# Performance work log

Measured on AMD Instinct MI355X. Metric: run time of the kernel, lower is better.

The kernel has to match this reference:

```python
import jax, jax.numpy as jnp
import numpy as np

B, T, N, M = 64, 128, 128, 512


def setup_inputs() -> dict:
    key = jax.random.key(0)
    ks = jax.random.split(key, 9)
    w = 0.02
    return dict(
        X=jax.random.normal(ks[0], (B, T, N), jnp.float32),
        h0=jax.random.normal(ks[1], (B, M), jnp.float32) * 0.05,
        s0=jax.random.normal(ks[2], (B, M), jnp.float32) * 0.05,
        # LSTM cell params (keras gate order: i, f, c, o)
        W_lstm=jax.random.normal(ks[3], (N, 4 * M), jnp.float32) * w,
        U_lstm=jax.random.normal(ks[4], (M, 4 * M), jnp.float32) * w,
        b_lstm=jnp.zeros((4 * M,), jnp.float32),
        # InputAttention params: W_e: Dense(T) on concat([h,c]) (2m -> T),
        # U_e: Dense(T) on X^T (T -> T), v_e: Dense(1) (T -> 1)
        W_e=jax.random.normal(ks[5], (2 * M, T), jnp.float32) * w,
        b_We=jnp.zeros((T,), jnp.float32),
        U_e=jax.random.normal(ks[6], (T, T), jnp.float32) * w,
        b_Ue=jnp.zeros((T,), jnp.float32),
        v_e=jax.random.normal(ks[7], (T, 1), jnp.float32) * w,
        b_ve=jnp.zeros((1,), jnp.float32),
    )


def reference(X, h0, s0, W_lstm, U_lstm, b_lstm, W_e, b_We, U_e, b_Ue, v_e, b_ve):
    # In the original, every loop iteration t runs a single LSTM step on
    # X[:, t, :] starting from the SAME initial_state [h0, s0] (state is not
    # carried across t), so all T steps are independent -> vectorize over T.
    z = jnp.einsum('btn,nk->btk', X, W_lstm) + (h0 @ U_lstm + b_lstm)[:, None, :]
    zi, zf, zc, zo = jnp.split(z, 4, axis=-1)  # keras gate order i,f,c,o
    i = jax.nn.sigmoid(zi)
    f = jax.nn.sigmoid(zf)
    o = jax.nn.sigmoid(zo)
    c = f * s0[:, None, :] + i * jnp.tanh(zc)  # (B, T, m)
    h = o * jnp.tanh(c)                        # (B, T, m)

    # InputAttention for every t at once:
    # e_t = v_e(tanh(W_e([h_t; c_t]) broadcast over n  +  U_e(X^T)))
    hc = jnp.concatenate([h, c], axis=-1)              # (B, T, 2m)
    A = hc @ W_e + b_We                                # (B, T, T)
    U = jnp.einsum('btn,tk->bnk', X, U_e) + b_Ue       # (B, n, T)
    e = jnp.tanh(A[:, :, None, :] + U[:, None, :, :])  # (B, T, n, T)
    scores = jnp.einsum('btnk,k->btn', e, v_e[:, 0]) + b_ve[0]  # (B, T, n)
    alpha = jax.nn.softmax(scores, axis=-1)            # softmax over n
    return X * alpha
```

## Files before the change

kernel.cpp:

```cpp
#include <hip/hip_runtime.h>

typedef __attribute__((ext_vector_type(8))) short bfrag;
typedef __attribute__((ext_vector_type(4))) float f32x4;

#define C_SCALE 2.885390081777926815f

__device__ __forceinline__ float fast_rcp(float x){
#if __has_builtin(__builtin_amdgcn_rcpf)
  return __builtin_amdgcn_rcpf(x);
#else
  return 1.0f/x;
#endif
}
__device__ __forceinline__ float fexp2(float x){
#if __has_builtin(__builtin_amdgcn_exp2f)
  return __builtin_amdgcn_exp2f(x);
#else
  return exp2f(x);
#endif
}
__device__ __forceinline__ float sigm(float x){ return fast_rcp(1.0f + __expf(-x)); }
__device__ __forceinline__ float tanh_f(float x){ return 1.0f - 2.0f*fast_rcp(__expf(2.0f*x) + 1.0f); }
__device__ __forceinline__ unsigned short f2bf(float f){
  unsigned u = __float_as_uint(f);
  return (unsigned short)((u + 0x7fffu + ((u>>16)&1u)) >> 16);
}
__device__ __forceinline__ void gload16(const void* g, void* l){
  __builtin_amdgcn_global_load_lds((const __attribute__((address_space(1))) void*)g,
                                   (__attribute__((address_space(3))) void*)l, 16, 0, 0);
}

__global__ __launch_bounds__(256) void prep(const float* __restrict__ X,
                                            unsigned short* __restrict__ Xbf,
                                            const float* __restrict__ Wl,
                                            unsigned short* __restrict__ Wlt,
                                            const float* __restrict__ We,
                                            unsigned short* __restrict__ Wet,
                                            const float* __restrict__ h0,
                                            const float* __restrict__ Ul,
                                            float* __restrict__ Uhp,
                                            const float* __restrict__ Ue,
                                            const float* __restrict__ bUe,
                                            unsigned short* __restrict__ UTb){
  __shared__ __align__(16) float sh[6600];
  const int tid = threadIdx.x;
  const int bid = blockIdx.x;

  if (bid < 512){
    const int i = (bid*256 + tid)*8;
    float4 a = *(const float4*)&X[i];
    float4 b = *(const float4*)&X[i+4];
    ushort4 lo, hi;
    lo.x=f2bf(a.x); lo.y=f2bf(a.y); lo.z=f2bf(a.z); lo.w=f2bf(a.w);
    hi.x=f2bf(b.x); hi.y=f2bf(b.y); hi.z=f2bf(b.z); hi.w=f2bf(b.w);
    *(ushort4*)&Xbf[i] = lo; *(ushort4*)&Xbf[i+4] = hi;
  } else if (bid < 608){
    const float* in; unsigned short* outp; int K, N, j0, k0, perm;
    if (bid < 576){ int r = bid-512; in = Wl; outp = Wlt; K = 128;  N = 2048; j0 = (r&31)*64; k0 = (r>>5)*64; perm = 0; }
    else          { int r = bid-576; in = We; outp = Wet; K = 1024; N = 128;  j0 = (r&1)*64;  k0 = (r>>1)*64; perm = 1; }
    float (*t)[68] = (float(*)[68])sh;
#pragma unroll
    for (int i=0;i<4;i++){
      int idx = tid + i*256;
      int r = idx>>4, c4 = idx&15;
      int kk = k0 + r;
      int srow = perm ? ((kk&1) ? 512 + (kk>>1) : (kk>>1)) : kk;
      *(float4*)&t[r][c4*4] = *(const float4*)&in[srow*N + j0 + c4*4];
    }
    __syncthreads();
#pragma unroll
    for (int i=0;i<4;i++){
      int idx = tid + i*256;
      int r = idx>>4, c4 = idx&15;
      ushort4 o;
      o.x = f2bf(t[c4*4+0][r]); o.y = f2bf(t[c4*4+1][r]);
      o.z = f2bf(t[c4*4+2][r]); o.w = f2bf(t[c4*4+3][r]);
      *(ushort4*)&outp[(j0+r)*K + k0 + c4*4] = o;
    }
  } else if (bid < 736){
    const int r = bid - 608;
    const int nh = r & 1, b = r >> 1;
    float (*Xs)[68]  = (float(*)[68])sh;
    float (*Us)[132] = (float(*)[132])(sh + 2176);
    const int tc5 = tid & 31, tr8 = tid >> 5;
    f32x4 a4[8];
#pragma unroll
    for (int j=0;j<8;j++) a4[j] = (f32x4){0.f,0.f,0.f,0.f};
    for (int tk=0; tk<4; tk++){
#pragma unroll
      for (int i=0;i<2;i++){
        int idx = tid + i*256;
        int t = idx>>4, nq = idx&15;
        *(float4*)&Xs[t][nq*4] = *(const float4*)&X[(b*128 + tk*32 + t)*128 + nh*64 + nq*4];
      }
#pragma unroll
      for (int i=0;i<4;i++){
        int idx = tid + i*256;
        int t = idx>>5, kq = idx&31;
        *(float4*)&Us[t][kq*4] = *(const float4*)&Ue[(tk*32+t)*128 + kq*4];
      }
      __syncthreads();
#pragma unroll 4
      for (int t=0;t<32;t++){
        f32x4 u4 = *(const f32x4*)&Us[t][tc5*4];
        f32x4 x0 = *(const f32x4*)&Xs[t][tr8*8];
        f32x4 x1 = *(const f32x4*)&Xs[t][tr8*8+4];
        a4[0] += x0.x*u4; a4[1] += x0.y*u4; a4[2] += x0.z*u4; a4[3] += x0.w*u4;
        a4[4] += x1.x*u4; a4[5] += x1.y*u4; a4[6] += x1.z*u4; a4[7] += x1.w*u4;
      }
      __syncthreads();
    }
    const f32x4 bu = *(const f32x4*)&bUe[tc5*4];
#pragma unroll
    for (int j=0;j<8;j++){
      const int n = nh*64 + tr8*8 + j;
      f32x4 v = a4[j] + bu;
      ushort4 o;
      o.x = f2bf(fexp2(C_SCALE*v.x)); o.y = f2bf(fexp2(C_SCALE*v.y));
      o.z = f2bf(fexp2(C_SCALE*v.z)); o.w = f2bf(fexp2(C_SCALE*v.w));
      *(ushort4*)&UTb[(b*128 + n)*128 + tc5*4] = o;
    }
  } else {
    const int r = bid - 736;
    const int jc = r & 15;
    const int bc = (r>>4) >> 2, kc = (r>>4) & 3;
    float (*h0s)[128] = (float(*)[128])sh;
#pragma unroll
    for (int i=0;i<2;i++){
      int idx = tid + i*256;
      int bi = idx>>5, kq = idx&31;
      *(float4*)&h0s[bi][kq*4] = *(const float4*)&h0[(bc*16+bi)*512 + kc*128 + kq*4];
    }
    __syncthreads();
    const int jj = tid & 127, bh = tid >> 7;
    const int j = jc*128 + jj;
    float acc[8];
#pragma unroll
    for (int i=0;i<8;i++) acc[i]=0.f;
    for (int k=0;k<128;k+=4){
      float w0 = Ul[(kc*128+k+0)*2048 + j];
      float w1 = Ul[(kc*128+k+1)*2048 + j];
      float w2 = Ul[(kc*128+k+2)*2048 + j];
      float w3 = Ul[(kc*128+k+3)*2048 + j];
#pragma unroll
      for (int bi=0;bi<8;bi++){
        float4 h4 = *(const float4*)&h0s[bh*8+bi][k];
        acc[bi] += h4.x*w0 + h4.y*w1 + h4.z*w2 + h4.w*w3;
      }
    }
#pragma unroll
    for (int bi=0;bi<8;bi++)
      Uhp[kc*131072 + (bc*16 + bh*8 + bi)*2048 + j] = acc[bi];
  }
}

__global__ __launch_bounds__(256) void k2_mfma(const unsigned short* __restrict__ Xbf,
                                               const unsigned short* __restrict__ Wlt,
                                               const float* __restrict__ Uhp,
                                               const float* __restrict__ bl,
                                               const float* __restrict__ s0,
                                               unsigned int* __restrict__ hci){
  __shared__ __align__(16) char lds[65536];
  const int tid = threadIdx.x;
  const int mc = blockIdx.x;
  const int b  = blockIdx.y;
  const int bt0 = b*128;
  const int lane = tid & 63, wave = tid >> 6;
  const int wr = wave >> 1, wc = wave & 1;

#pragma unroll
  for (int i=0;i<8;i++){
    int g = tid + i*256;
    int r = g>>4, G = g&15;
    gload16(Xbf + (bt0+r)*128 + ((G ^ (r&7))<<3), lds + g*16);
  }
#pragma unroll
  for (int i=0;i<8;i++){
    int g = tid + i*256;
    int c = g>>4, G = g&15;
    int q = c>>4;
    int j = (q&3)*512 + mc*32 + ((q>>2)<<4) + (c&15);
    gload16(Wlt + j*128 + ((G ^ (c&7))<<3), lds + 32768 + g*16);
  }
  __syncthreads();

  f32x4 acc[4][4];
#pragma unroll
  for (int mt=0;mt<4;mt++)
#pragma unroll
    for (int nt=0;nt<4;nt++) acc[mt][nt] = (f32x4){0.f,0.f,0.f,0.f};

#pragma unroll
  for (int ks=0;ks<4;ks++){
    const int kb = ks*64 + ((lane>>4)<<4);
    bfrag a[4], bb[4];
#pragma unroll
    for (int mt=0;mt<4;mt++){
      int r = wr*64 + mt*16 + (lane&15);
      a[mt] = *(const bfrag*)&lds[r*256 + (kb ^ ((r&7)<<4))];
    }
#pragma unroll
    for (int nt=0;nt<4;nt++){
      int c = wc*64 + nt*16 + (lane&15);
      bb[nt] = *(const bfrag*)&lds[32768 + c*256 + (kb ^ ((c&7)<<4))];
    }
#pragma unroll
    for (int mt=0;mt<4;mt++)
#pragma unroll
      for (int nt=0;nt<4;nt++)
        acc[mt][nt] = __builtin_amdgcn_mfma_f32_16x16x32_bf16(a[mt], bb[nt], acc[mt][nt], 0, 0, 0);
  }

  const int mloc = mc*32 + wc*16 + (lane&15);
  float uh[4];
#pragma unroll
  for (int g=0;g<4;g++){
    int j = g*512 + mloc;
    uh[g] = bl[j] + Uhp[0*131072 + b*2048 + j] + Uhp[1*131072 + b*2048 + j]
                  + Uhp[2*131072 + b*2048 + j] + Uhp[3*131072 + b*2048 + j];
  }
  const float s0v = s0[b*512 + mloc];
#pragma unroll
  for (int mt=0;mt<4;mt++){
#pragma unroll
    for (int reg=0;reg<4;reg++){
      int row = wr*64 + mt*16 + (lane>>4)*4 + reg;
      float zi = acc[mt][0][reg] + uh[0];
      float zf = acc[mt][1][reg] + uh[1];
      float zc = acc[mt][2][reg] + uh[2];
      float zo = acc[mt][3][reg] + uh[3];
      float fi = sigm(zi), ff = sigm(zf), fo = sigm(zo);
      float cv = ff*s0v + fi*tanh_f(zc);
      float hv = fo*tanh_f(cv);
      hci[(bt0+row)*512 + mloc] = (unsigned)f2bf(hv) | ((unsigned)f2bf(cv) << 16);
    }
  }
}

__global__ __launch_bounds__(256) void k3_mfma(const unsigned short* __restrict__ hc,
                                               const unsigned short* __restrict__ Wet,
                                               const float* __restrict__ bWe,
                                               float* __restrict__ eA){
  __shared__ __align__(16) char lds[49152];
  const int tid = threadIdx.x;
  const int rc = blockIdx.x;
  const int bt0 = rc*64;
  const int lane = tid & 63, wave = tid >> 6;
  const int wr = wave >> 1, wc = wave & 1;

  f32x4 acc[2][4];
#pragma unroll
  for (int mt=0;mt<2;mt++)
#pragma unroll
    for (int nt=0;nt<4;nt++) acc[mt][nt] = (f32x4){0.f,0.f,0.f,0.f};

  for (int ks=0; ks<8; ks++){
    const int k0 = ks*128;
#pragma unroll
    for (int i=0;i<4;i++){
      int g = tid + i*256;
      int r = g>>4, G = g&15;
      gload16(hc + (bt0+r)*1024 + k0 + ((G ^ (r&7))<<3), lds + g*16);
    }
#pragma unroll
    for (int i=0;i<8;i++){
      int g = tid + i*256;
      int nn = g>>4, G = g&15;
      gload16(Wet + nn*1024 + k0 + ((G ^ (nn&7))<<3), lds + 16384 + g*16);
    }
    __syncthreads();
#pragma unroll
    for (int kk=0;kk<4;kk++){
      const int kb = kk*64 + ((lane>>4)<<4);
      bfrag a[2], bb[4];
#pragma unroll
      for (int mt=0;mt<2;mt++){
        int r = wr*32 + mt*16 + (lane&15);
        a[mt] = *(const bfrag*)&lds[r*256 + (kb ^ ((r&7)<<4))];
      }
#pragma unroll
      for (int nt=0;nt<4;nt++){
        int nn = wc*64 + nt*16 + (lane&15);
        bb[nt] = *(const bfrag*)&lds[16384 + nn*256 + (kb ^ ((nn&7)<<4))];
      }
#pragma unroll
      for (int mt=0;mt<2;mt++)
#pragma unroll
        for (int nt=0;nt<4;nt++)
          acc[mt][nt] = __builtin_amdgcn_mfma_f32_16x16x32_bf16(a[mt], bb[nt], acc[mt][nt], 0, 0, 0);
    }
    __syncthreads();
  }
#pragma unroll
  for (int mt=0;mt<2;mt++)
#pragma unroll
    for (int reg=0;reg<4;reg++){
      int row = wr*32 + mt*16 + (lane>>4)*4 + reg;
#pragma unroll
      for (int nt=0;nt<4;nt++){
        int col = wc*64 + nt*16 + (lane&15);
        eA[(bt0+row)*128 + col] = fexp2(C_SCALE*(acc[mt][nt][reg] + bWe[col]));
      }
    }
}

__global__ __launch_bounds__(256) void k5_score(const float* __restrict__ X,
                                                const unsigned short* __restrict__ UTb,
                                                const float* __restrict__ eA,
                                                const float* __restrict__ ve,
                                                float* __restrict__ out){
  __shared__ __align__(16) unsigned short Un[128*128];
  __shared__ __align__(16) float As[8*128];
  __shared__ __align__(16) float vs[128];
  __shared__ float redm[4][4], reds[4][4];
  const int tid = threadIdx.x;
  const int tch = blockIdx.x;
  const int b   = blockIdx.y;
  const int tpair = tid>>7, n = tid&127, wid = tid>>6;

  {
    const unsigned short* src = UTb + b*16384;
#pragma unroll
    for (int i=0;i<8;i++){
      int g = tid + i*256;
      int nn = g>>4, G = g&15;
      gload16(src + nn*128 + ((G ^ (nn&7))<<3), (char*)Un + g*16);
    }
    const float* asrc = eA + (b*128 + tch*8)*128;
    gload16(asrc + tid*4, (char*)As + tid*16);
    if (tid < 128) vs[tid] = ve[tid];
  }
  __syncthreads();

  f32x4 sc[4];
#pragma unroll
  for (int tt=0;tt<4;tt++) sc[tt] = (f32x4){0.f,0.f,0.f,0.f};

  const char* Urow = (const char*)Un + n*256;
  const int swz = (n&7)<<4;
#pragma unroll 4
  for (int k8=0; k8<16; k8++){
    uint4 u = *(const uint4*)(Urow + ((k8*16) ^ swz));
    f32x4 ua, ub;
    ua.x = __uint_as_float(u.x<<16); ua.y = __uint_as_float(u.x & 0xffff0000u);
    ua.z = __uint_as_float(u.y<<16); ua.w = __uint_as_float(u.y & 0xffff0000u);
    ub.x = __uint_as_float(u.z<<16); ub.y = __uint_as_float(u.z & 0xffff0000u);
    ub.z = __uint_as_float(u.w<<16); ub.w = __uint_as_float(u.w & 0xffff0000u);
    const f32x4 va = *(const f32x4*)&vs[k8*8];
    const f32x4 vb = *(const f32x4*)&vs[k8*8+4];
#pragma unroll
    for (int tt=0; tt<4; tt++){
      const float* Ar = &As[(tt*2+tpair)*128 + k8*8];
      f32x4 ea = *(const f32x4*)Ar;
      f32x4 eb = *(const f32x4*)(Ar+4);
      f32x4 ra, rb;
      ra.x = fast_rcp(ea.x*ua.x + 1.f); ra.y = fast_rcp(ea.y*ua.y + 1.f);
      ra.z = fast_rcp(ea.z*ua.z + 1.f); ra.w = fast_rcp(ea.w*ua.w + 1.f);
      rb.x = fast_rcp(eb.x*ub.x + 1.f); rb.y = fast_rcp(eb.y*ub.y + 1.f);
      rb.z = fast_rcp(eb.z*ub.z + 1.f); rb.w = fast_rcp(eb.w*ub.w + 1.f);
      sc[tt] += va*ra;
      sc[tt] += vb*rb;
    }
  }

  float sv[4];
#pragma unroll
  for (int tt=0;tt<4;tt++){
    float s = -2.f*((sc[tt].x + sc[tt].y) + (sc[tt].z + sc[tt].w));
    sv[tt] = s;
    float m = s;
#pragma unroll
    for (int off=32; off>0; off>>=1) m = fmaxf(m, __shfl_xor(m, off));
    if ((tid&63)==0) redm[wid][tt] = m;
  }
  __syncthreads();
  float evv[4];
#pragma unroll
  for (int tt=0;tt<4;tt++){
    const float M = fmaxf(redm[tpair*2][tt], redm[tpair*2+1][tt]);
    float e = __expf(sv[tt] - M);
    evv[tt] = e;
    float s = e;
#pragma unroll
    for (int off=32; off>0; off>>=1) s += __shfl_xor(s, off);
    if ((tid&63)==0) reds[wid][tt] = s;
  }
  __syncthreads();
#pragma unroll
  for (int tt=0;tt<4;tt++){
    const float S = reds[tpair*2][tt] + reds[tpair*2+1][tt];
    const float alpha = evv[tt] * fast_rcp(S);
    const int t = tch*8 + tt*2 + tpair;
    const int g = (b*128 + t)*128 + n;
    out[g] = X[g] * alpha;
  }
}

extern "C" void kernel_launch(void* const* d_in, const int* in_sizes, int n_in,
                              void* d_out, int out_size, void* d_ws, size_t ws_size,
                              hipStream_t stream){
  (void)in_sizes; (void)n_in; (void)out_size; (void)ws_size;
  const float* X   = (const float*)d_in[0];
  const float* h0  = (const float*)d_in[1];
  const float* s0  = (const float*)d_in[2];
  const float* Wl  = (const float*)d_in[3];
  const float* Ul  = (const float*)d_in[4];
  const float* bl  = (const float*)d_in[5];
  const float* We  = (const float*)d_in[6];
  const float* bWe = (const float*)d_in[7];
  const float* Ue  = (const float*)d_in[8];
  const float* bUe = (const float*)d_in[9];
  const float* ve  = (const float*)d_in[10];
  float* out = (float*)d_out;

  char* ws = (char*)d_ws;
  unsigned short* Wlt = (unsigned short*)(ws + 0);
  unsigned short* Wet = (unsigned short*)(ws + 524288);
  unsigned short* Xbf = (unsigned short*)(ws + 786432);
  unsigned short* UTb = (unsigned short*)(ws + 2883584);
  unsigned short* hc  = (unsigned short*)(ws + 4980736);
  float*          Uhp = (float*)(ws + 21757952);
  float*          eA  = (float*)(ws + 23855104);

  prep    <<<dim3(992),   256, 0, stream>>>(X, Xbf, Wl, Wlt, We, Wet, h0, Ul, Uhp, Ue, bUe, UTb);
  k2_mfma <<<dim3(16,64), 256, 0, stream>>>(Xbf, Wlt, Uhp, bl, s0, (unsigned int*)hc);
  k3_mfma <<<dim3(128),   256, 0, stream>>>(hc, Wet, bWe, eA);
  k5_score<<<dim3(16,64), 256, 0, stream>>>(X, UTb, eA, ve, out);
}
```

Before: 67.68 us.

## Shrink LDS footprints, split k3 tiles, retile UTb for direct global reads

k2 now stages the K dimension in two 64-wide halves, halving its LDS use, and launches on a flattened 1D grid. k3 is split into 512 smaller blocks, each computing a 32x64 output tile, so more blocks run across CUs. UTb is written in a k-tiled layout so k5 can read it with coalesced loads straight from global memory, dropping its 32KB LDS staging. The aim is higher occupancy and less LDS staging; the costs are extra barriers in k2, more redundant loads of hc and Wet in k3, and k5 now depending on cache hits for the repeated UTb reads.

```diff
diff --git a/kernel.cpp b/kernel.cpp
--- a/kernel.cpp
+++ b/kernel.cpp
@@ -111,6 +111,7 @@
       __syncthreads();
     }
     const f32x4 bu = *(const f32x4*)&bUe[tc5*4];
+    const int ktile = tc5 >> 1, khalf = tc5 & 1;
 #pragma unroll
     for (int j=0;j<8;j++){
       const int n = nh*64 + tr8*8 + j;
@@ -118,7 +119,7 @@
       ushort4 o;
       o.x = f2bf(fexp2(C_SCALE*v.x)); o.y = f2bf(fexp2(C_SCALE*v.y));
       o.z = f2bf(fexp2(C_SCALE*v.z)); o.w = f2bf(fexp2(C_SCALE*v.w));
-      *(ushort4*)&UTb[(b*128 + n)*128 + tc5*4] = o;
+      *(ushort4*)&UTb[b*16384 + ktile*1024 + n*8 + khalf*4] = o;
     }
   } else {
     const int r = bid - 736;
@@ -154,61 +155,62 @@
   }
 }
 
-__global__ __launch_bounds__(256) void k2_mfma(const unsigned short* __restrict__ Xbf,
-                                               const unsigned short* __restrict__ Wlt,
-                                               const float* __restrict__ Uhp,
-                                               const float* __restrict__ bl,
-                                               const float* __restrict__ s0,
-                                               unsigned int* __restrict__ hci){
-  __shared__ __align__(16) char lds[65536];
+__global__ __launch_bounds__(256) void k2_k(const unsigned short* __restrict__ Xbf,
+                                            const unsigned short* __restrict__ Wlt,
+                                            const float* __restrict__ Uhp,
+                                            const float* __restrict__ bl,
+                                            const float* __restrict__ s0,
+                                            unsigned int* __restrict__ hci){
+  __shared__ __align__(16) char lds[32768];
   const int tid = threadIdx.x;
-  const int mc = blockIdx.x;
-  const int b  = blockIdx.y;
+  const int mc = blockIdx.x & 15, b = blockIdx.x >> 4;
   const int bt0 = b*128;
   const int lane = tid & 63, wave = tid >> 6;
   const int wr = wave >> 1, wc = wave & 1;
 
-#pragma unroll
-  for (int i=0;i<8;i++){
-    int g = tid + i*256;
-    int r = g>>4, G = g&15;
-    gload16(Xbf + (bt0+r)*128 + ((G ^ (r&7))<<3), lds + g*16);
-  }
-#pragma unroll
-  for (int i=0;i<8;i++){
-    int g = tid + i*256;
-    int c = g>>4, G = g&15;
-    int q = c>>4;
-    int j = (q&3)*512 + mc*32 + ((q>>2)<<4) + (c&15);
-    gload16(Wlt + j*128 + ((G ^ (c&7))<<3), lds + 32768 + g*16);
-  }
-  __syncthreads();
-
   f32x4 acc[4][4];
 #pragma unroll
   for (int mt=0;mt<4;mt++)
 #pragma unroll
     for (int nt=0;nt<4;nt++) acc[mt][nt] = (f32x4){0.f,0.f,0.f,0.f};
 
-#pragma unroll
-  for (int ks=0;ks<4;ks++){
-    const int kb = ks*64 + ((lane>>4)<<4);
-    bfrag a[4], bb[4];
-#pragma unroll
-    for (int mt=0;mt<4;mt++){
-      int r = wr*64 + mt*16 + (lane&15);
-      a[mt] = *(const bfrag*)&lds[r*256 + (kb ^ ((r&7)<<4))];
-    }
-#pragma unroll
-    for (int nt=0;nt<4;nt++){
-      int c = wc*64 + nt*16 + (lane&15);
-      bb[nt] = *(const bfrag*)&lds[32768 + c*256 + (kb ^ ((c&7)<<4))];
-    }
-#pragma unroll
-    for (int mt=0;mt<4;mt++)
-#pragma unroll
-      for (int nt=0;nt<4;nt++)
-        acc[mt][nt] = __builtin_amdgcn_mfma_f32_16x16x32_bf16(a[mt], bb[nt], acc[mt][nt], 0, 0, 0);
+  for (int kh=0; kh<2; kh++){
+#pragma unroll
+    for (int i=0;i<4;i++){
+      int g = tid + i*256;
+      int r = g>>3, G = g&7;
+      gload16(Xbf + (bt0+r)*128 + kh*64 + ((G ^ (r&7))<<3), lds + g*16);
+    }
+#pragma unroll
+    for (int i=0;i<4;i++){
+      int g = tid + i*256;
+      int c = g>>3, G = g&7;
+      int q = c>>4;
+      int j = (q&3)*512 + mc*32 + ((q>>2)<<4) + (c&15);
+      gload16(Wlt + j*128 + kh*64 + ((G ^ (c&7))<<3), lds + 16384 + g*16);
+    }
+    __syncthreads();
+#pragma unroll
+    for (int ks2=0; ks2<2; ks2++){
+      const int kb = ks2*64 + ((lane>>4)<<4);
+      bfrag a[4], bb[4];
+#pragma unroll
+      for (int mt=0;mt<4;mt++){
+        int r = wr*64 + mt*16 + (lane&15);
+        a[mt] = *(const bfrag*)&lds[r*128 + (kb ^ ((r&7)<<4))];
+      }
+#pragma unroll
+      for (int nt=0;nt<4;nt++){
+        int c = wc*64 + nt*16 + (lane&15);
+        bb[nt] = *(const bfrag*)&lds[16384 + c*128 + (kb ^ ((c&7)<<4))];
+      }
+#pragma unroll
+      for (int mt=0;mt<4;mt++)
+#pragma unroll
+        for (int nt=0;nt<4;nt++)
+          acc[mt][nt] = __builtin_amdgcn_mfma_f32_16x16x32_bf16(a[mt], bb[nt], acc[mt][nt], 0, 0, 0);
+    }
+    __syncthreads();
   }
 
   const int mloc = mc*32 + wc*16 + (lane&15);
@@ -237,79 +239,69 @@
   }
 }
 
-__global__ __launch_bounds__(256) void k3_mfma(const unsigned short* __restrict__ hc,
-                                               const unsigned short* __restrict__ Wet,
-                                               const float* __restrict__ bWe,
-                                               float* __restrict__ eA){
-  __shared__ __align__(16) char lds[49152];
+__global__ __launch_bounds__(256) void k3_k(const unsigned short* __restrict__ hc,
+                                            const unsigned short* __restrict__ Wet,
+                                            const float* __restrict__ bWe,
+                                            float* __restrict__ eA){
+  __shared__ __align__(16) char lds[24576];
+  const int nc = blockIdx.x & 1, rc = blockIdx.x >> 1;
+  const int bt0 = rc*32;
   const int tid = threadIdx.x;
-  const int rc = blockIdx.x;
-  const int bt0 = rc*64;
   const int lane = tid & 63, wave = tid >> 6;
   const int wr = wave >> 1, wc = wave & 1;
 
-  f32x4 acc[2][4];
-#pragma unroll
-  for (int mt=0;mt<2;mt++)
-#pragma unroll
-    for (int nt=0;nt<4;nt++) acc[mt][nt] = (f32x4){0.f,0.f,0.f,0.f};
+  f32x4 acc[2];
+  acc[0] = (f32x4){0.f,0.f,0.f,0.f};
+  acc[1] = (f32x4){0.f,0.f,0.f,0.f};
 
   for (int ks=0; ks<8; ks++){
     const int k0 = ks*128;
+#pragma unroll
+    for (int i=0;i<2;i++){
+      int g = tid + i*256;
+      int r = g>>4, G = g&15;
+      gload16(hc + (bt0+r)*1024 + k0 + ((G ^ (r&7))<<3), lds + g*16);
+    }
 #pragma unroll
     for (int i=0;i<4;i++){
       int g = tid + i*256;
       int r = g>>4, G = g&15;
-      gload16(hc + (bt0+r)*1024 + k0 + ((G ^ (r&7))<<3), lds + g*16);
-    }
-#pragma unroll
-    for (int i=0;i<8;i++){
-      int g = tid + i*256;
-      int nn = g>>4, G = g&15;
-      gload16(Wet + nn*1024 + k0 + ((G ^ (nn&7))<<3), lds + 16384 + g*16);
+      gload16(Wet + (nc*64 + r)*1024 + k0 + ((G ^ (r&7))<<3), lds + 8192 + g*16);
     }
     __syncthreads();
 #pragma unroll
     for (int kk=0;kk<4;kk++){
       const int kb = kk*64 + ((lane>>4)<<4);
-      bfrag a[2], bb[4];
-#pragma unroll
-      for (int mt=0;mt<2;mt++){
-        int r = wr*32 + mt*16 + (lane&15);
-        a[mt] = *(const bfrag*)&lds[r*256 + (kb ^ ((r&7)<<4))];
-      }
-#pragma unroll
-      for (int nt=0;nt<4;nt++){
-        int nn = wc*64 + nt*16 + (lane&15);
-        bb[nt] = *(const bfrag*)&lds[16384 + nn*256 + (kb ^ ((nn&7)<<4))];
-      }
-#pragma unroll
-      for (int mt=0;mt<2;mt++)
-#pragma unroll
-        for (int nt=0;nt<4;nt++)
-          acc[mt][nt] = __builtin_amdgcn_mfma_f32_16x16x32_bf16(a[mt], bb[nt], acc[mt][nt], 0, 0, 0);
-    }
-    __syncthreads();
-  }
-#pragma unroll
-  for (int mt=0;mt<2;mt++)
-#pragma unroll
-    for (int reg=0;reg<4;reg++){
-      int row = wr*32 + mt*16 + (lane>>4)*4 + reg;
-#pragma unroll
-      for (int nt=0;nt<4;nt++){
-        int col = wc*64 + nt*16 + (lane&15);
-        eA[(bt0+row)*128 + col] = fexp2(C_SCALE*(acc[mt][nt][reg] + bWe[col]));
-      }
-    }
-}
-
-__global__ __launch_bounds__(256) void k5_score(const float* __restrict__ X,
-                                                const unsigned short* __restrict__ UTb,
-                                                const float* __restrict__ eA,
-                                                const float* __restrict__ ve,
-                                                float* __restrict__ out){
-  __shared__ __align__(16) unsigned short Un[128*128];
+      int r = wr*16 + (lane&15);
+      bfrag a = *(const bfrag*)&lds[r*256 + (kb ^ ((r&7)<<4))];
+      bfrag bb0, bb1;
+      {
+        int nn = wc*32 + 0*16 + (lane&15);
+        bb0 = *(const bfrag*)&lds[8192 + nn*256 + (kb ^ ((nn&7)<<4))];
+        nn = wc*32 + 1*16 + (lane&15);
+        bb1 = *(const bfrag*)&lds[8192 + nn*256 + (kb ^ ((nn&7)<<4))];
+      }
+      acc[0] = __builtin_amdgcn_mfma_f32_16x16x32_bf16(a, bb0, acc[0], 0, 0, 0);
+      acc[1] = __builtin_amdgcn_mfma_f32_16x16x32_bf16(a, bb1, acc[1], 0, 0, 0);
+    }
+    __syncthreads();
+  }
+#pragma unroll
+  for (int reg=0; reg<4; reg++){
+    int row = bt0 + wr*16 + (lane>>4)*4 + reg;
+#pragma unroll
+    for (int nt=0;nt<2;nt++){
+      int col = nc*64 + wc*32 + nt*16 + (lane&15);
+      eA[row*128 + col] = fexp2(C_SCALE*(acc[nt][reg] + bWe[col]));
+    }
+  }
+}
+
+__global__ __launch_bounds__(256) void k5_k(const float* __restrict__ X,
+                                            const unsigned short* __restrict__ UTb,
+                                            const float* __restrict__ eA,
+                                            const float* __restrict__ ve,
+                                            float* __restrict__ out){
   __shared__ __align__(16) float As[8*128];
   __shared__ __align__(16) float vs[128];
   __shared__ float redm[4][4], reds[4][4];
@@ -319,13 +311,6 @@
   const int tpair = tid>>7, n = tid&127, wid = tid>>6;
 
   {
-    const unsigned short* src = UTb + b*16384;
-#pragma unroll
-    for (int i=0;i<8;i++){
-      int g = tid + i*256;
-      int nn = g>>4, G = g&15;
-      gload16(src + nn*128 + ((G ^ (nn&7))<<3), (char*)Un + g*16);
-    }
     const float* asrc = eA + (b*128 + tch*8)*128;
     gload16(asrc + tid*4, (char*)As + tid*16);
     if (tid < 128) vs[tid] = ve[tid];
@@ -336,11 +321,10 @@
 #pragma unroll
   for (int tt=0;tt<4;tt++) sc[tt] = (f32x4){0.f,0.f,0.f,0.f};
 
-  const char* Urow = (const char*)Un + n*256;
-  const int swz = (n&7)<<4;
+  const unsigned short* urow = UTb + b*16384 + n*8;
 #pragma unroll 4
   for (int k8=0; k8<16; k8++){
-    uint4 u = *(const uint4*)(Urow + ((k8*16) ^ swz));
+    uint4 u = *(const uint4*)(urow + k8*1024);
     f32x4 ua, ub;
     ua.x = __uint_as_float(u.x<<16); ua.y = __uint_as_float(u.x & 0xffff0000u);
     ua.z = __uint_as_float(u.y<<16); ua.w = __uint_as_float(u.y & 0xffff0000u);
@@ -421,9 +405,10 @@
   unsigned short* hc  = (unsigned short*)(ws + 4980736);
   float*          Uhp = (float*)(ws + 21757952);
   float*          eA  = (float*)(ws + 23855104);
-
-  prep    <<<dim3(992),   256, 0, stream>>>(X, Xbf, Wl, Wlt, We, Wet, h0, Ul, Uhp, Ue, bUe, UTb);
-  k2_mfma <<<dim3(16,64), 256, 0, stream>>>(Xbf, Wlt, Uhp, bl, s0, (unsigned int*)hc);
-  k3_mfma <<<dim3(128),   256, 0, stream>>>(hc, Wet, bWe, eA);
-  k5_score<<<dim3(16,64), 256, 0, stream>>>(X, UTb, eA, ve, out);
-}
+  unsigned int*   hci = (unsigned int*)hc;
+
+  prep <<<dim3(992),    256, 0, stream>>>(X, Xbf, Wl, Wlt, We, Wet, h0, Ul, Uhp, Ue, bUe, UTb);
+  k2_k <<<dim3(1024),   256, 0, stream>>>(Xbf, Wlt, Uhp, bl, s0, hci);
+  k3_k <<<dim3(512),    256, 0, stream>>>(hc, Wet, bWe, eA);
+  k5_k <<<dim3(16,64),  256, 0, stream>>>(X, UTb, eA, ve, out);
+}
```

Result: faster. 61.97 us (median of 3 runs) (-8.4%).
